# Performance work log

Hardware: AMD Instinct MI355X
Metric: run time of the kernel (lower is better)

## Reference

```python
import jax, jax.numpy as jnp
import numpy as np

B, S, E, H = 4, 2048, 1024, 16
HD = E // H  # head_dim = 64
EPS = 1.1920928955078125e-07  # torch.finfo(float32).eps (RMSNorm eps=None default)


def _rmsnorm(x, w):
    # normalize over last dim
    ms = jnp.mean(x * x, axis=-1, keepdims=True)
    return x * jax.lax.rsqrt(ms + EPS) * w


def _rope(x, start_pos=0):
    # x: [B, H, S, HD]; interleaved (even/odd) rotary embedding
    seq_len = x.shape[-2]
    inv_freq = 1.0 / (10000.0 ** (jnp.arange(0, HD, 2, dtype=jnp.float32) / HD))  # [HD/2]
    t = jnp.arange(start_pos, start_pos + seq_len, dtype=jnp.float32)  # [S]
    freqs = t[:, None] * inv_freq[None, :]  # [S, HD/2]
    cos = jnp.cos(freqs)[None, None]  # [1,1,S,HD/2]
    sin = jnp.sin(freqs)[None, None]
    x1 = x[..., 0::2]
    x2 = x[..., 1::2]
    o1 = x1 * cos - x2 * sin
    o2 = x1 * sin + x2 * cos
    # stack(..., -1).flatten(-2) -> re-interleave
    return jnp.stack((o1, o2), axis=-1).reshape(x.shape)


def setup_inputs() -> dict:
    key = jax.random.key(0)
    k1, k2, k3, k4 = jax.random.split(key, 4)
    lim = 1.0 / np.sqrt(E)
    return {
        "q": jax.random.normal(k1, (B, S, E), jnp.float32),
        "k": jax.random.normal(k2, (B, S, E), jnp.float32),
        "v": jax.random.normal(k3, (B, S, E), jnp.float32),
        "q_norm_w": jnp.ones((HD,), jnp.float32),
        "k_norm_w": jnp.ones((HD,), jnp.float32),
        "proj_w": jax.random.uniform(k4, (E, E), jnp.float32, -lim, lim),
        "proj_b": jnp.zeros((E,), jnp.float32),
    }


def reference(q, k, v, q_norm_w, k_norm_w, proj_w, proj_b):
    b, s, _ = q.shape
    scale = HD ** -0.5
    # [B,S,E] -> [B,H,S,HD]
    qh = q.reshape(b, s, H, HD).transpose(0, 2, 1, 3)
    kh = k.reshape(b, s, H, HD).transpose(0, 2, 1, 3)
    vh = v.reshape(b, s, H, HD).transpose(0, 2, 1, 3)
    # per-head QK RMSNorm then RoPE
    qh = _rope(_rmsnorm(qh, q_norm_w))
    kh = _rope(_rmsnorm(kh, k_norm_w))
    # explicit attention (no mask path)
    scores = jnp.einsum("bhqd,bhkd->bhqk", qh, kh) * scale  # [B,H,S,S]
    attn = jax.nn.softmax(scores, axis=-1)
    ctx = jnp.einsum("bhqk,bhkd->bhqd", attn, vh)
    ctx = ctx.transpose(0, 2, 1, 3).reshape(b, s, E)
    return ctx @ proj_w.T + proj_b
```

## Files before the change

kernel.cpp:

```cpp
#include <hip/hip_runtime.h>
#include <hip/hip_bf16.h>
#include <cstdint>

#define B_ 4
#define S_ 2048
#define E_ 1024
#define H_ 16
#define HD_ 64
#define EPS_ 1.1920928955078125e-07f

typedef __attribute__((ext_vector_type(8))) short shortx8;
typedef __attribute__((ext_vector_type(4))) float floatx4;
typedef __attribute__((ext_vector_type(8))) _Float16 halfx8;
typedef __attribute__((ext_vector_type(2))) __fp16 fp16x2;

#define C1_ 0.18033688068389154f

__global__ __launch_bounds__(256) void prep(
    const float* __restrict__ q, const float* __restrict__ k,
    const float* __restrict__ v,
    const float* __restrict__ qw, const float* __restrict__ kw,
    const float* __restrict__ pw,
    __hip_bfloat16* __restrict__ qh, __hip_bfloat16* __restrict__ kh,
    _Float16* __restrict__ vt, __hip_bfloat16* __restrict__ wb)
{
    __shared__ _Float16 tile[64][72];
    const int bid = blockIdx.x;
    const int tid = threadIdx.x;

    if (bid < 16384) {
        const size_t PT = (size_t)B_ * S_ * E_ / 4;
        size_t t = (size_t)bid * 256 + tid;
        const bool is_k = (t >= PT);
        if (is_k) t -= PT;

        const int row = (int)(t >> 8);
        const int b   = row / S_;
        const int s   = row % S_;
        const int grp = (int)(t & 255);
        const int h   = grp >> 4;
        const int dl  = (grp & 15) * 4;

        const float* __restrict__ src = is_k ? k : q;
        const float* __restrict__ w   = is_k ? kw : qw;
        __hip_bfloat16* __restrict__ dst = is_k ? kh : qh;

        const float4 x  = ((const float4*)src)[t];
        const float4 wv = ((const float4*)w)[grp & 15];

        float ss = x.x * x.x + x.y * x.y + x.z * x.z + x.w * x.w;
#pragma unroll
        for (int m = 1; m < 16; m <<= 1) ss += __shfl_xor(ss, m);
        float r = rsqrtf(ss * (1.0f / HD_) + EPS_);
        if (!is_k) r *= C1_;

        const float xn0 = x.x * r * wv.x;
        const float xn1 = x.y * r * wv.y;
        const float xn2 = x.z * r * wv.z;
        const float xn3 = x.w * r * wv.w;

        const float L2I = 0.41524101186092029f;
        const int   i0  = dl >> 1;
        const float f0  = (float)s * __builtin_amdgcn_exp2f(-(float)i0 * L2I);
        const float f1  = (float)s * __builtin_amdgcn_exp2f(-(float)(i0 + 1) * L2I);
        const float c0 = __cosf(f0), sn0 = __sinf(f0);
        const float c1 = __cosf(f1), sn1 = __sinf(f1);

        __hip_bfloat16 pk[4];
        pk[0] = __float2bfloat16(xn0 * c0 - xn1 * sn0);
        pk[1] = __float2bfloat16(xn0 * sn0 + xn1 * c0);
        pk[2] = __float2bfloat16(xn2 * c1 - xn3 * sn1);
        pk[3] = __float2bfloat16(xn2 * sn1 + xn3 * c1);
        *(ushort4*)(dst + ((size_t)((b * H_ + h) * S_ + s)) * HD_ + dl) =
            *(const ushort4*)pk;
    } else if (bid < 18432) {
        const int bb2 = bid - 16384;
        const int s0  = (bb2 & 31) * 64;
        const int bh  = bb2 >> 5;
        const int b   = bh >> 4, h = bh & 15;
        {
            const int sl = tid >> 2;
            const int o  = sl;
            const int n  = (o & 32) | (((o >> 2) & 3) << 3) |
                           (((o >> 4) & 1) << 2) | (o & 3);
            const int d0 = (tid & 3) * 16;
            const float* __restrict__ src =
                v + ((size_t)(b * S_ + s0 + sl)) * E_ + h * HD_ + d0;
            float4 f0 = ((const float4*)src)[0];
            float4 f1 = ((const float4*)src)[1];
            float4 f2 = ((const float4*)src)[2];
            float4 f3 = ((const float4*)src)[3];
            float vals[16] = {f0.x,f0.y,f0.z,f0.w, f1.x,f1.y,f1.z,f1.w,
                              f2.x,f2.y,f2.z,f2.w, f3.x,f3.y,f3.z,f3.w};
#pragma unroll
            for (int j = 0; j < 16; ++j)
                tile[d0 + j][n] = (_Float16)vals[j];
        }
        __syncthreads();
        {
            const int d  = tid >> 2;
            const int sg = (tid & 3) * 16;
            _Float16* __restrict__ dst =
                vt + ((size_t)(bh * HD_ + d)) * S_ + s0 + sg;
            ((uint4*)dst)[0] = *(const uint4*)&tile[d][sg];
            ((uint4*)dst)[1] = *(const uint4*)&tile[d][sg + 8];
        }
    } else {
        const int i = (bid - 18432) * 256 + tid;
        float4 f = ((const float4*)pw)[i];
        wb[4 * i + 0] = __float2bfloat16(f.x);
        wb[4 * i + 1] = __float2bfloat16(f.y);
        wb[4 * i + 2] = __float2bfloat16(f.z);
        wb[4 * i + 3] = __float2bfloat16(f.w);
    }
}

__global__ __launch_bounds__(256, 2) void attn(
    const __hip_bfloat16* __restrict__ qh, const __hip_bfloat16* __restrict__ kh,
    const _Float16* __restrict__ vt, __hip_bfloat16* __restrict__ ctx)
{
    __shared__ __hip_bfloat16 Kt[128][72];
    __shared__ _Float16       Vt[64][152];

    const int bid  = blockIdx.x;
    const int slot = bid >> 3;
    const int bh   = ((bid & 7) << 3) | (slot & 7);
    const int q0   = (slot >> 3) * 256;
    const int tid  = threadIdx.x;
    const int wv   = tid >> 6;
    const int lane = tid & 63;
    const int l16  = lane & 15;
    const int quad = lane >> 4;
    const int b    = bh >> 4, h = bh & 15;

    shortx8 aq[4][2];
#pragma unroll
    for (int mh = 0; mh < 4; ++mh) {
        const __hip_bfloat16* qbase =
            qh + ((size_t)bh * S_ + q0 + wv * 64 + mh * 16 + l16) * HD_;
        aq[mh][0] = *(const shortx8*)(qbase + quad * 8);
        aq[mh][1] = *(const shortx8*)(qbase + 32 + quad * 8);
    }

    const halfx8 ones = {(_Float16)1.f, (_Float16)1.f, (_Float16)1.f, (_Float16)1.f,
                         (_Float16)1.f, (_Float16)1.f, (_Float16)1.f, (_Float16)1.f};

    floatx4 O[4][4] = {};
    floatx4 O5[4]   = {};

    const __hip_bfloat16* __restrict__ kbase = kh + (size_t)bh * S_ * HD_;
    const _Float16* __restrict__ vbase = vt + (size_t)bh * HD_ * S_;

    const int sr = tid >> 1, sc = (tid & 1) * 32;
    const int vr = tid >> 2, vc = (tid & 3) * 32;

    for (int kt = 0; kt < S_ / 128; ++kt) {
        {
            const __hip_bfloat16* kp = kbase + ((size_t)(kt * 128 + sr)) * HD_ + sc;
            uint4 k0 = ((const uint4*)kp)[0];
            uint4 k1 = ((const uint4*)kp)[1];
            uint4 k2 = ((const uint4*)kp)[2];
            uint4 k3 = ((const uint4*)kp)[3];
            *(uint4*)&Kt[sr][sc]      = k0;
            *(uint4*)&Kt[sr][sc + 8]  = k1;
            *(uint4*)&Kt[sr][sc + 16] = k2;
            *(uint4*)&Kt[sr][sc + 24] = k3;
            const _Float16* vp = vbase + (size_t)vr * S_ + kt * 128 + vc;
            uint4 v0 = ((const uint4*)vp)[0];
            uint4 v1 = ((const uint4*)vp)[1];
            uint4 v2 = ((const uint4*)vp)[2];
            uint4 v3 = ((const uint4*)vp)[3];
            *(uint4*)&Vt[vr][vc]      = v0;
            *(uint4*)&Vt[vr][vc + 8]  = v1;
            *(uint4*)&Vt[vr][vc + 16] = v2;
            *(uint4*)&Vt[vr][vc + 24] = v3;
        }
        __syncthreads();

#pragma unroll
        for (int hk = 0; hk < 2; ++hk) {
            floatx4 s4[4][4];
#pragma unroll
            for (int nt = 0; nt < 4; ++nt) {
                const shortx8 kb0 =
                    *(const shortx8*)&Kt[hk * 64 + nt * 16 + l16][quad * 8];
                const shortx8 kb1 =
                    *(const shortx8*)&Kt[hk * 64 + nt * 16 + l16][32 + quad * 8];
#pragma unroll
                for (int mh = 0; mh < 4; ++mh) {
                    floatx4 c = {0.f, 0.f, 0.f, 0.f};
                    c = __builtin_amdgcn_mfma_f32_16x16x32_bf16(kb0, aq[mh][0], c, 0, 0, 0);
                    c = __builtin_amdgcn_mfma_f32_16x16x32_bf16(kb1, aq[mh][1], c, 0, 0, 0);
                    s4[mh][nt] = c;
                }
            }

            halfx8 bb[4][2];
#pragma unroll
            for (int mh = 0; mh < 4; ++mh)
#pragma unroll
                for (int f = 0; f < 2; ++f) {
                    union { fp16x2 h2[4]; halfx8 h8; } u;
                    u.h2[0] = __builtin_amdgcn_cvt_pkrtz(
                        __builtin_amdgcn_exp2f(s4[mh][2 * f][0]),
                        __builtin_amdgcn_exp2f(s4[mh][2 * f][1]));
                    u.h2[1] = __builtin_amdgcn_cvt_pkrtz(
                        __builtin_amdgcn_exp2f(s4[mh][2 * f][2]),
                        __builtin_amdgcn_exp2f(s4[mh][2 * f][3]));
                    u.h2[2] = __builtin_amdgcn_cvt_pkrtz(
                        __builtin_amdgcn_exp2f(s4[mh][2 * f + 1][0]),
                        __builtin_amdgcn_exp2f(s4[mh][2 * f + 1][1]));
                    u.h2[3] = __builtin_amdgcn_cvt_pkrtz(
                        __builtin_amdgcn_exp2f(s4[mh][2 * f + 1][2]),
                        __builtin_amdgcn_exp2f(s4[mh][2 * f + 1][3]));
                    bb[mh][f] = u.h8;
                }

#pragma unroll
            for (int mh = 0; mh < 4; ++mh) {
                O5[mh] = __builtin_amdgcn_mfma_f32_16x16x32_f16(ones, bb[mh][0], O5[mh], 0, 0, 0);
                O5[mh] = __builtin_amdgcn_mfma_f32_16x16x32_f16(ones, bb[mh][1], O5[mh], 0, 0, 0);
            }

#pragma unroll
            for (int dt = 0; dt < 4; ++dt) {
                const _Float16* vrow = &Vt[dt * 16 + l16][hk * 64];
                const halfx8 A0 = *(const halfx8*)(vrow + quad * 8);
                const halfx8 A1 = *(const halfx8*)(vrow + 32 + quad * 8);
#pragma unroll
                for (int mh = 0; mh < 4; ++mh) {
                    O[mh][dt] = __builtin_amdgcn_mfma_f32_16x16x32_f16(
                        A0, bb[mh][0], O[mh][dt], 0, 0, 0);
                    O[mh][dt] = __builtin_amdgcn_mfma_f32_16x16x32_f16(
                        A1, bb[mh][1], O[mh][dt], 0, 0, 0);
                }
            }
        }
        __syncthreads();
    }

#pragma unroll
    for (int mh = 0; mh < 4; ++mh) {
        const float inv = 1.0f / O5[mh][0];
        const int s = q0 + wv * 64 + mh * 16 + l16;
        __hip_bfloat16* cb = ctx + ((size_t)(b * S_ + s)) * E_ + h * HD_;
#pragma unroll
        for (int dt = 0; dt < 4; ++dt) {
            __hip_bfloat16 pk[4];
#pragma unroll
            for (int r = 0; r < 4; ++r)
                pk[r] = __float2bfloat16(O[mh][dt][r] * inv);
            *(ushort4*)(cb + dt * 16 + quad * 4) = *(const ushort4*)pk;
        }
    }
}

__global__ __launch_bounds__(256) void proj(
    const __hip_bfloat16* __restrict__ ctx, const __hip_bfloat16* __restrict__ wb,
    const float* __restrict__ bias, float* __restrict__ out)
{
    __shared__ __hip_bfloat16 As[128][72];
    __shared__ __hip_bfloat16 Bs[128][72];

    const int bid  = blockIdx.x;
    const int slot = bid >> 3;
    const int mblk = ((bid & 7) << 3) | (slot & 7);
    const int nblk = slot >> 3;
    const int m0 = mblk * 128;
    const int n0 = nblk * 128;
    const int tid  = threadIdx.x;
    const int wv   = tid >> 6;
    const int lane = tid & 63;
    const int l16  = lane & 15;
    const int quad = lane >> 4;
    const int wr   = (wv >> 1) * 64;
    const int wc   = (wv & 1) * 64;

    const int srow = tid >> 1;
    const int scol = (tid & 1) * 32;

    floatx4 acc[4][4] = {};

    for (int k0 = 0; k0 < E_; k0 += 64) {
        const uint4* ap = (const uint4*)(ctx + (size_t)(m0 + srow) * E_ + k0 + scol);
        const uint4* bp = (const uint4*)(wb  + (size_t)(n0 + srow) * E_ + k0 + scol);
        uint4 a0 = ap[0], a1 = ap[1], a2 = ap[2], a3 = ap[3];
        uint4 b0 = bp[0], b1 = bp[1], b2 = bp[2], b3 = bp[3];
        *(uint4*)&As[srow][scol]      = a0;
        *(uint4*)&As[srow][scol + 8]  = a1;
        *(uint4*)&As[srow][scol + 16] = a2;
        *(uint4*)&As[srow][scol + 24] = a3;
        *(uint4*)&Bs[srow][scol]      = b0;
        *(uint4*)&Bs[srow][scol + 8]  = b1;
        *(uint4*)&Bs[srow][scol + 16] = b2;
        *(uint4*)&Bs[srow][scol + 24] = b3;
        __syncthreads();

#pragma unroll
        for (int ks = 0; ks < 2; ++ks) {
            shortx8 af[4], bf[4];
#pragma unroll
            for (int mt = 0; mt < 4; ++mt)
                af[mt] = *(const shortx8*)&As[wr + mt * 16 + l16][ks * 32 + quad * 8];
#pragma unroll
            for (int nt = 0; nt < 4; ++nt)
                bf[nt] = *(const shortx8*)&Bs[wc + nt * 16 + l16][ks * 32 + quad * 8];

#pragma unroll
            for (int mt = 0; mt < 4; ++mt)
#pragma unroll
                for (int nt = 0; nt < 4; ++nt)
                    acc[mt][nt] = __builtin_amdgcn_mfma_f32_16x16x32_bf16(
                        af[mt], bf[nt], acc[mt][nt], 0, 0, 0);
        }
        __syncthreads();
    }

#pragma unroll
    for (int nt = 0; nt < 4; ++nt) {
        const float bv = bias[n0 + wc + nt * 16 + l16];
#pragma unroll
        for (int mt = 0; mt < 4; ++mt)
#pragma unroll
            for (int r = 0; r < 4; ++r) {
                const int mrow = m0 + wr + mt * 16 + quad * 4 + r;
                const int ncol = n0 + wc + nt * 16 + l16;
                out[(size_t)mrow * E_ + ncol] = acc[mt][nt][r] + bv;
            }
    }
}

extern "C" void kernel_launch(void* const* d_in, const int* in_sizes, int n_in,
                              void* d_out, int out_size, void* d_ws, size_t ws_size,
                              hipStream_t stream)
{
    const float* q  = (const float*)d_in[0];
    const float* k  = (const float*)d_in[1];
    const float* v  = (const float*)d_in[2];
    const float* qw = (const float*)d_in[3];
    const float* kw = (const float*)d_in[4];
    const float* pw = (const float*)d_in[5];
    const float* pb = (const float*)d_in[6];
    float* out = (float*)d_out;

    char* ws = (char*)d_ws;
    const size_t SEG = (size_t)B_ * H_ * S_ * HD_ * 2;
    __hip_bfloat16* qh  = (__hip_bfloat16*)(ws);
    __hip_bfloat16* kh  = (__hip_bfloat16*)(ws + SEG);
    _Float16*       vt  = (_Float16*)(ws + 2 * SEG);
    __hip_bfloat16* ctx = (__hip_bfloat16*)(ws + 3 * SEG);
    __hip_bfloat16* wbp = (__hip_bfloat16*)(ws + 4 * SEG);

    prep<<<dim3(19456), 256, 0, stream>>>(q, k, v, qw, kw, pw, qh, kh, vt, wbp);
    attn<<<dim3(512), 256, 0, stream>>>(qh, kh, vt, ctx);
    proj<<<dim3(512), 256, 0, stream>>>(ctx, wbp, pb, out);
}
```

Measured before the change: 246.0 us.

## Halve attention query tile, prefetch next K/V tile into registers, add MFMA priority

Each attention block now handles 128 query rows instead of 256, and the grid doubles to 1024 blocks with launch bounds raised to 4 blocks per SM. This gives more parallelism and occupancy across the CUs. The next K and V tiles are loaded from global memory into registers while the current tile is being computed, so load latency overlaps with the MFMA work. s_setprio is raised around the MFMA sections. The trade-off is that each K/V tile loaded into LDS is reused by fewer query rows, which doubles K/V global traffic, and the prefetch registers add pressure.

```diff
diff --git a/kernel.cpp b/kernel.cpp
--- a/kernel.cpp
+++ b/kernel.cpp
@@ -115,7 +115,7 @@
     }
 }
 
-__global__ __launch_bounds__(256, 2) void attn(
+__global__ __launch_bounds__(256, 4) void attn(
     const __hip_bfloat16* __restrict__ qh, const __hip_bfloat16* __restrict__ kh,
     const _Float16* __restrict__ vt, __hip_bfloat16* __restrict__ ctx)
 {
@@ -125,7 +125,7 @@
     const int bid  = blockIdx.x;
     const int slot = bid >> 3;
     const int bh   = ((bid & 7) << 3) | (slot & 7);
-    const int q0   = (slot >> 3) * 256;
+    const int q0   = (slot >> 3) * 128;
     const int tid  = threadIdx.x;
     const int wv   = tid >> 6;
     const int lane = tid & 63;
@@ -133,11 +133,11 @@
     const int quad = lane >> 4;
     const int b    = bh >> 4, h = bh & 15;
 
-    shortx8 aq[4][2];
-#pragma unroll
-    for (int mh = 0; mh < 4; ++mh) {
+    shortx8 aq[2][2];
+#pragma unroll
+    for (int mh = 0; mh < 2; ++mh) {
         const __hip_bfloat16* qbase =
-            qh + ((size_t)bh * S_ + q0 + wv * 64 + mh * 16 + l16) * HD_;
+            qh + ((size_t)bh * S_ + q0 + wv * 32 + mh * 16 + l16) * HD_;
         aq[mh][0] = *(const shortx8*)(qbase + quad * 8);
         aq[mh][1] = *(const shortx8*)(qbase + 32 + quad * 8);
     }
@@ -145,8 +145,8 @@
     const halfx8 ones = {(_Float16)1.f, (_Float16)1.f, (_Float16)1.f, (_Float16)1.f,
                          (_Float16)1.f, (_Float16)1.f, (_Float16)1.f, (_Float16)1.f};
 
-    floatx4 O[4][4] = {};
-    floatx4 O5[4]   = {};
+    floatx4 O[2][4] = {};
+    floatx4 O5[2]   = {};
 
     const __hip_bfloat16* __restrict__ kbase = kh + (size_t)bh * S_ * HD_;
     const _Float16* __restrict__ vbase = vt + (size_t)bh * HD_ * S_;
@@ -154,32 +154,35 @@
     const int sr = tid >> 1, sc = (tid & 1) * 32;
     const int vr = tid >> 2, vc = (tid & 3) * 32;
 
+    uint4 gk0, gk1, gk2, gk3, gv0, gv1, gv2, gv3;
+    {
+        const uint4* kp = (const uint4*)(kbase + (size_t)sr * HD_ + sc);
+        gk0 = kp[0]; gk1 = kp[1]; gk2 = kp[2]; gk3 = kp[3];
+        const uint4* vp = (const uint4*)(vbase + (size_t)vr * S_ + vc);
+        gv0 = vp[0]; gv1 = vp[1]; gv2 = vp[2]; gv3 = vp[3];
+    }
+
     for (int kt = 0; kt < S_ / 128; ++kt) {
-        {
-            const __hip_bfloat16* kp = kbase + ((size_t)(kt * 128 + sr)) * HD_ + sc;
-            uint4 k0 = ((const uint4*)kp)[0];
-            uint4 k1 = ((const uint4*)kp)[1];
-            uint4 k2 = ((const uint4*)kp)[2];
-            uint4 k3 = ((const uint4*)kp)[3];
-            *(uint4*)&Kt[sr][sc]      = k0;
-            *(uint4*)&Kt[sr][sc + 8]  = k1;
-            *(uint4*)&Kt[sr][sc + 16] = k2;
-            *(uint4*)&Kt[sr][sc + 24] = k3;
-            const _Float16* vp = vbase + (size_t)vr * S_ + kt * 128 + vc;
-            uint4 v0 = ((const uint4*)vp)[0];
-            uint4 v1 = ((const uint4*)vp)[1];
-            uint4 v2 = ((const uint4*)vp)[2];
-            uint4 v3 = ((const uint4*)vp)[3];
-            *(uint4*)&Vt[vr][vc]      = v0;
-            *(uint4*)&Vt[vr][vc + 8]  = v1;
-            *(uint4*)&Vt[vr][vc + 16] = v2;
-            *(uint4*)&Vt[vr][vc + 24] = v3;
-        }
-        __syncthreads();
+        *(uint4*)&Kt[sr][sc]      = gk0;
+        *(uint4*)&Kt[sr][sc + 8]  = gk1;
+        *(uint4*)&Kt[sr][sc + 16] = gk2;
+        *(uint4*)&Kt[sr][sc + 24] = gk3;
+        *(uint4*)&Vt[vr][vc]      = gv0;
+        *(uint4*)&Vt[vr][vc + 8]  = gv1;
+        *(uint4*)&Vt[vr][vc + 16] = gv2;
+        *(uint4*)&Vt[vr][vc + 24] = gv3;
+        __syncthreads();
+
+        if (kt + 1 < S_ / 128) {
+            const uint4* kp = (const uint4*)(kbase +
+                (size_t)((kt + 1) * 128 + sr) * HD_ + sc);
+            gk0 = kp[0]; gk1 = kp[1]; gk2 = kp[2]; gk3 = kp[3];
+        }
 
 #pragma unroll
         for (int hk = 0; hk < 2; ++hk) {
-            floatx4 s4[4][4];
+            floatx4 s4[2][4];
+            __builtin_amdgcn_s_setprio(1);
 #pragma unroll
             for (int nt = 0; nt < 4; ++nt) {
                 const shortx8 kb0 =
@@ -187,17 +190,18 @@
                 const shortx8 kb1 =
                     *(const shortx8*)&Kt[hk * 64 + nt * 16 + l16][32 + quad * 8];
 #pragma unroll
-                for (int mh = 0; mh < 4; ++mh) {
+                for (int mh = 0; mh < 2; ++mh) {
                     floatx4 c = {0.f, 0.f, 0.f, 0.f};
                     c = __builtin_amdgcn_mfma_f32_16x16x32_bf16(kb0, aq[mh][0], c, 0, 0, 0);
                     c = __builtin_amdgcn_mfma_f32_16x16x32_bf16(kb1, aq[mh][1], c, 0, 0, 0);
                     s4[mh][nt] = c;
                 }
             }
-
-            halfx8 bb[4][2];
-#pragma unroll
-            for (int mh = 0; mh < 4; ++mh)
+            __builtin_amdgcn_s_setprio(0);
+
+            halfx8 bb[2][2];
+#pragma unroll
+            for (int mh = 0; mh < 2; ++mh)
 #pragma unroll
                 for (int f = 0; f < 2; ++f) {
                     union { fp16x2 h2[4]; halfx8 h8; } u;
@@ -216,8 +220,15 @@
                     bb[mh][f] = u.h8;
                 }
 
-#pragma unroll
-            for (int mh = 0; mh < 4; ++mh) {
+            if (hk == 0 && kt + 1 < S_ / 128) {
+                const uint4* vp = (const uint4*)(vbase +
+                    (size_t)vr * S_ + (kt + 1) * 128 + vc);
+                gv0 = vp[0]; gv1 = vp[1]; gv2 = vp[2]; gv3 = vp[3];
+            }
+
+            __builtin_amdgcn_s_setprio(1);
+#pragma unroll
+            for (int mh = 0; mh < 2; ++mh) {
                 O5[mh] = __builtin_amdgcn_mfma_f32_16x16x32_f16(ones, bb[mh][0], O5[mh], 0, 0, 0);
                 O5[mh] = __builtin_amdgcn_mfma_f32_16x16x32_f16(ones, bb[mh][1], O5[mh], 0, 0, 0);
             }
@@ -228,21 +239,22 @@
                 const halfx8 A0 = *(const halfx8*)(vrow + quad * 8);
                 const halfx8 A1 = *(const halfx8*)(vrow + 32 + quad * 8);
 #pragma unroll
-                for (int mh = 0; mh < 4; ++mh) {
+                for (int mh = 0; mh < 2; ++mh) {
                     O[mh][dt] = __builtin_amdgcn_mfma_f32_16x16x32_f16(
                         A0, bb[mh][0], O[mh][dt], 0, 0, 0);
                     O[mh][dt] = __builtin_amdgcn_mfma_f32_16x16x32_f16(
                         A1, bb[mh][1], O[mh][dt], 0, 0, 0);
                 }
             }
-        }
-        __syncthreads();
-    }
-
-#pragma unroll
-    for (int mh = 0; mh < 4; ++mh) {
+            __builtin_amdgcn_s_setprio(0);
+        }
+        __syncthreads();
+    }
+
+#pragma unroll
+    for (int mh = 0; mh < 2; ++mh) {
         const float inv = 1.0f / O5[mh][0];
-        const int s = q0 + wv * 64 + mh * 16 + l16;
+        const int s = q0 + wv * 32 + mh * 16 + l16;
         __hip_bfloat16* cb = ctx + ((size_t)(b * S_ + s)) * E_ + h * HD_;
 #pragma unroll
         for (int dt = 0; dt < 4; ++dt) {
@@ -352,6 +364,6 @@
     __hip_bfloat16* wbp = (__hip_bfloat16*)(ws + 4 * SEG);
 
     prep<<<dim3(19456), 256, 0, stream>>>(q, k, v, qw, kw, pw, qh, kh, vt, wbp);
-    attn<<<dim3(512), 256, 0, stream>>>(qh, kh, vt, ctx);
+    attn<<<dim3(1024), 256, 0, stream>>>(qh, kh, vt, ctx);
     proj<<<dim3(512), 256, 0, stream>>>(ctx, wbp, pb, out);
 }
```

Result: slower. 273.1 us (+11.0%).
